# Kernel tuning notes

Measured on AMD Instinct MI355X. Metric: run time of the kernel, lower is better.

## Reference

```python
import jax, jax.numpy as jnp
import numpy as np
from functools import partial

B, D, E, O, K = 65536, 64, 16, 512, 2  # batch, feat dim, num_experts, output_size, top-k


def setup_inputs() -> dict:
    key = jax.random.key(0)
    k1, k2, k3, k4, k5 = jax.random.split(key, 5)
    scale_g = 1.0 / np.sqrt(D)
    return {
        "x": jax.random.normal(k1, (B, D), dtype=jnp.float32),
        "wg": jax.random.uniform(k2, (D, E), dtype=jnp.float32, minval=-scale_g, maxval=scale_g),
        "bg": jnp.zeros((E,), dtype=jnp.float32),
        "We": jax.random.uniform(k3, (E, D, O), dtype=jnp.float32, minval=-scale_g, maxval=scale_g),
        "be": jax.random.uniform(k4, (E, O), dtype=jnp.float32, minval=-scale_g, maxval=scale_g),
    }


def reference(x, wg, bg, We, be):
    # --- gating (noisy_gating=False / eval path) ---
    logits = jax.nn.softmax(x @ wg + bg, axis=1)            # [B, E]
    top_vals, top_idx = jax.lax.top_k(logits, K)            # [B, K]
    top_gates = top_vals / (jnp.sum(top_vals, axis=1, keepdims=True) + 1e-6)
    rows = jnp.arange(x.shape[0])[:, None]                  # [B, 1]
    gates = jnp.zeros_like(logits).at[rows, top_idx].set(top_gates)  # dense [B, E], sparse rows

    # --- dispatch / per-expert linear / gated scatter-combine ---
    # Equivalent dense-masked form of SparseDispatcher: y[i] = sum_e gates[i,e] * (x[i] @ We[e] + be[e])
    def step(y, ewb):
        w, b, g = ewb                                       # [D,O], [O], [B]
        return y + g[:, None] * (x @ w + b), None

    y0 = jnp.zeros((x.shape[0], We.shape[2]), dtype=x.dtype)
    y, _ = jax.lax.scan(step, y0, (We, be, gates.T))
    return y
```

## Files before the change

kernel.cpp:

```cpp
#include <hip/hip_runtime.h>

typedef unsigned int u32;
typedef unsigned short u16;
typedef float f4 __attribute__((ext_vector_type(4)));
typedef __bf16 b8 __attribute__((ext_vector_type(8)));
typedef unsigned short us8 __attribute__((ext_vector_type(8)));

#define DD 64
#define NE 16
#define OO 512
#define TR 64
#define MAXT 1344

struct __align__(16) Tile { u32 pid, slot, nr, pad; };

union U8 { us8 u; b8 b; };

__device__ __forceinline__ u16 f2bf(float f) {
  u32 u = __float_as_uint(f);
  u32 r = (u + 0x7fffu + ((u >> 16) & 1u)) >> 16;
  return (u16)r;
}

__global__ void k_wt(const float* __restrict__ We, u16* __restrict__ WeT) {
  __shared__ float tl[64][65];
  int b = blockIdx.x;
  int e = b >> 3;
  int oc = (b & 7) * 64;
  int t = threadIdx.x;
  int d = t >> 2, seg = (t & 3) * 16;
  const f4* src = (const f4*)(We + ((size_t)(e * DD + d)) * OO + oc + seg);
  f4 v0 = src[0], v1 = src[1], v2 = src[2], v3 = src[3];
#pragma unroll
  for (int j = 0; j < 4; j++) {
    tl[d][seg + j]      = v0[j];
    tl[d][seg + 4 + j]  = v1[j];
    tl[d][seg + 8 + j]  = v2[j];
    tl[d][seg + 12 + j] = v3[j];
  }
  __syncthreads();
  int o = t >> 2, ds = (t & 3) * 16;
  us8 o0, o1;
#pragma unroll
  for (int j = 0; j < 8; j++) {
    o0[j] = f2bf(tl[ds + j][o]);
    o1[j] = f2bf(tl[ds + 8 + j][o]);
  }
  u16* dst = WeT + ((size_t)(e * OO + oc + o)) * DD + ds;
  *(us8*)dst = o0;
  *(us8*)(dst + 8) = o1;
}

__global__ void k_gate(const float* __restrict__ x, const float* __restrict__ wg,
                       const float* __restrict__ bg, u32* __restrict__ hist,
                       u32* __restrict__ pid_arr, float* __restrict__ glo_arr,
                       float* __restrict__ ghi_arr) {
  __shared__ u32 hcnt[256];
  int t = threadIdx.x;
  hcnt[t] = 0;
  __syncthreads();
  int row = blockIdx.x * 256 + t;

  float l[NE];
#pragma unroll
  for (int e = 0; e < NE; e++) l[e] = bg[e];

  const f4* xp = (const f4*)(x + (size_t)row * DD);
  for (int d4 = 0; d4 < 16; d4++) {
    f4 xv = xp[d4];
#pragma unroll
    for (int qq = 0; qq < 4; qq++) {
      float xs = xv[qq];
      const float* wrow = wg + (d4 * 4 + qq) * NE;
#pragma unroll
      for (int e = 0; e < NE; e++) l[e] = fmaf(xs, wrow[e], l[e]);
    }
  }
  float mx = l[0];
#pragma unroll
  for (int e = 1; e < NE; e++) mx = fmaxf(mx, l[e]);
  float Z = 0.f;
#pragma unroll
  for (int e = 0; e < NE; e++) Z += __expf(l[e] - mx);
  int i1 = 0; float b1 = l[0];
#pragma unroll
  for (int e = 1; e < NE; e++) { if (l[e] > b1) { b1 = l[e]; i1 = e; } }
  int i2 = -1; float b2 = -1e30f;
#pragma unroll
  for (int e = 0; e < NE; e++) { if (e != i1 && l[e] > b2) { b2 = l[e]; i2 = e; } }
  float p1 = __expf(b1 - mx) / Z;
  float p2 = __expf(b2 - mx) / Z;
  float den = p1 + p2 + 1e-6f;
  float g1 = p1 / den, g2 = p2 / den;
  int elo, ehi; float glo, ghi;
  if (i1 < i2) { elo = i1; ehi = i2; glo = g1; ghi = g2; }
  else         { elo = i2; ehi = i1; glo = g2; ghi = g1; }
  u32 pid = (u32)(elo * NE + ehi);
  pid_arr[row] = pid;
  glo_arr[row] = glo;
  ghi_arr[row] = ghi;
  atomicAdd(&hcnt[pid], 1u);
  __syncthreads();
  hist[blockIdx.x * 256 + t] = hcnt[t];
}

__global__ void k_scan(u32* __restrict__ hist, u32* __restrict__ ntp,
                       Tile* __restrict__ tiles) {
  __shared__ u32 s[256], s2[256];
  int t = threadIdx.x;
  u32 total = 0;
  for (int b = 0; b < 256; b++) total += hist[b * 256 + t];
  u32 nt = (total + (TR - 1)) >> 6;
  s[t] = total; s2[t] = nt;
  __syncthreads();
  for (int d = 1; d < 256; d <<= 1) {
    u32 a = 0, c = 0;
    if (t >= d) { a = s[t - d]; c = s2[t - d]; }
    __syncthreads();
    s[t] += a; s2[t] += c;
    __syncthreads();
  }
  u32 base = s[t] - total;
  u32 tb   = s2[t] - nt;
  u32 run = base;
  for (int b = 0; b < 256; b++) {
    u32 v = hist[b * 256 + t];
    hist[b * 256 + t] = run;
    run += v;
  }
  for (u32 k = 0; k < nt; k++) {
    Tile td;
    td.pid = (u32)t;
    td.slot = base + k * (u32)TR;
    u32 rem = total - k * (u32)TR;
    td.nr = rem < (u32)TR ? rem : (u32)TR;
    td.pad = 0;
    tiles[tb + k] = td;
  }
  if (t == 255) *ntp = s2[255];
}

__global__ void k_scatter(const u32* __restrict__ pid_arr, const u32* __restrict__ hist,
                          u32* __restrict__ sorted) {
  __shared__ u32 lcnt[256];
  int t = threadIdx.x;
  lcnt[t] = 0;
  __syncthreads();
  int row = blockIdx.x * 256 + t;
  u32 pid = pid_arr[row];
  u32 rank = atomicAdd(&lcnt[pid], 1u);
  u32 off = hist[blockIdx.x * 256 + pid];
  sorted[off + rank] = (u32)row;
}

__global__ void k_moe(const float* __restrict__ x, const u16* __restrict__ WeT,
                      const float* __restrict__ be, const u32* __restrict__ sorted,
                      const u32* __restrict__ ntp, const Tile* __restrict__ tiles,
                      const float* __restrict__ glo_arr, const float* __restrict__ ghi_arr,
                      float* __restrict__ y) {
  __shared__ __align__(16) u16 Xl[TR * 72];
  __shared__ __align__(16) float Yl[TR * 68];
  __shared__ u32 rid_s[TR];
  __shared__ float glo_s[TR], ghi_s[TR];

  u32 bid = blockIdx.x;
  if (bid >= *ntp) return;
  Tile td = tiles[bid];
  u32 e_lo = td.pid >> 4, e_hi = td.pid & 15u;
  u32 slot0 = td.slot, nr = td.nr;

  int t = threadIdx.x;
  if (t < TR) {
    u32 i = (u32)t;
    u32 slot = slot0 + ((i < nr) ? i : 0u);
    u32 r = sorted[slot];
    rid_s[t] = r;
    bool valid = i < nr;
    glo_s[t] = valid ? glo_arr[r] : 0.f;
    ghi_s[t] = valid ? ghi_arr[r] : 0.f;
  }
  __syncthreads();
  {
    int i = t >> 2;
    int seg = (t & 3) * 16;
    u32 r = rid_s[i];
    const f4* xp = (const f4*)(x + (size_t)r * DD + seg);
    f4 v0 = xp[0], v1 = xp[1], v2 = xp[2], v3 = xp[3];
    float vv[16] = { v0[0], v0[1], v0[2], v0[3], v1[0], v1[1], v1[2], v1[3],
                     v2[0], v2[1], v2[2], v2[3], v3[0], v3[1], v3[2], v3[3] };
    us8 o0, o1;
#pragma unroll
    for (int j = 0; j < 8; j++) { o0[j] = f2bf(vv[j]); o1[j] = f2bf(vv[8 + j]); }
    *(us8*)&Xl[i * 72 + seg] = o0;
    *(us8*)&Xl[i * 72 + seg + 8] = o1;
  }
  __syncthreads();

  int lane = t & 63;
  int w = t >> 6;
  int q = lane >> 4;
  int ln = lane & 15;

  b8 afr[4][2];
#pragma unroll
  for (int mt = 0; mt < 4; mt++)
#pragma unroll
    for (int kc = 0; kc < 2; kc++) {
      U8 tmp; tmp.u = *(const us8*)&Xl[(mt * 16 + ln) * 72 + kc * 32 + q * 8];
      afr[mt][kc] = tmp.b;
    }

  float gl[16], gh[16];
#pragma unroll
  for (int mt = 0; mt < 4; mt++)
#pragma unroll
    for (int rr = 0; rr < 4; rr++) {
      int i = mt * 16 + q * 4 + rr;
      gl[mt * 4 + rr] = glo_s[i];
      gh[mt * 4 + rr] = ghi_s[i];
    }

  const u16* wlo = WeT + (size_t)e_lo * OO * DD;
  const u16* whi = WeT + (size_t)e_hi * OO * DD;
  const f4 zero = {0.f, 0.f, 0.f, 0.f};

  for (int jj = 0; jj < 8; jj++) {
    int col = jj * 64 + w * 16 + ln;
    const us8* plo = (const us8*)(wlo + (size_t)col * DD + q * 8);
    const us8* phi = (const us8*)(whi + (size_t)col * DD + q * 8);
    U8 t0, t1, t2, t3;
    t0.u = plo[0]; t1.u = plo[4];
    t2.u = phi[0]; t3.u = phi[4];
    b8 bl0 = t0.b, bl1 = t1.b, bh0 = t2.b, bh1 = t3.b;
    float blo = be[e_lo * OO + col];
    float bhi = be[e_hi * OO + col];

    f4 aL[4], aH[4];
#pragma unroll
    for (int mt = 0; mt < 4; mt++) { aL[mt] = zero; aH[mt] = zero; }
#pragma unroll
    for (int mt = 0; mt < 4; mt++) {
      aL[mt] = __builtin_amdgcn_mfma_f32_16x16x32_bf16(afr[mt][0], bl0, aL[mt], 0, 0, 0);
      aL[mt] = __builtin_amdgcn_mfma_f32_16x16x32_bf16(afr[mt][1], bl1, aL[mt], 0, 0, 0);
      aH[mt] = __builtin_amdgcn_mfma_f32_16x16x32_bf16(afr[mt][0], bh0, aH[mt], 0, 0, 0);
      aH[mt] = __builtin_amdgcn_mfma_f32_16x16x32_bf16(afr[mt][1], bh1, aH[mt], 0, 0, 0);
    }
#pragma unroll
    for (int mt = 0; mt < 4; mt++)
#pragma unroll
      for (int rr = 0; rr < 4; rr++) {
        int i = mt * 16 + q * 4 + rr;
        int idx = mt * 4 + rr;
        float v = gl[idx] * (aL[mt][rr] + blo) + gh[idx] * (aH[mt][rr] + bhi);
        Yl[i * 68 + w * 16 + ln] = v;
      }
    __syncthreads();
    {
      int row = t >> 2;
      int cs = (t & 3) * 16;
      if ((u32)row < nr) {
        float* yp = y + (size_t)rid_s[row] * OO + jj * 64 + cs;
        const float* sp = &Yl[row * 68 + cs];
#pragma unroll
        for (int u2 = 0; u2 < 4; u2++)
          *(f4*)(yp + u2 * 4) = *(const f4*)(sp + u2 * 4);
      }
    }
    __syncthreads();
  }
}

extern "C" void kernel_launch(void* const* d_in, const int* in_sizes, int n_in,
                              void* d_out, int out_size, void* d_ws, size_t ws_size,
                              hipStream_t stream) {
  const float* x  = (const float*)d_in[0];
  const float* wg = (const float*)d_in[1];
  const float* bg = (const float*)d_in[2];
  const float* We = (const float*)d_in[3];
  const float* be = (const float*)d_in[4];
  float* y = (float*)d_out;

  char* ws = (char*)d_ws;
  u32* ntp     = (u32*)(ws + 2048);
  Tile* tiles  = (Tile*)(ws + 4096);
  u32* pid_arr = (u32*)(ws + 32768);
  float* glo_a = (float*)(ws + 32768 + 262144);
  float* ghi_a = (float*)(ws + 32768 + 2 * 262144);
  u32* sorted  = (u32*)(ws + 32768 + 3 * 262144);
  u16* WeT     = (u16*)(ws + 32768 + 4 * 262144);
  u32* hist    = (u32*)(ws + 32768 + 4 * 262144 + 1048576);

  k_wt<<<128, 256, 0, stream>>>(We, WeT);
  k_gate<<<256, 256, 0, stream>>>(x, wg, bg, hist, pid_arr, glo_a, ghi_a);
  k_scan<<<1, 256, 0, stream>>>(hist, ntp, tiles);
  k_scatter<<<256, 256, 0, stream>>>(pid_arr, hist, sorted);
  k_moe<<<1144, 256, 0, stream>>>(x, WeT, be, sorted, ntp, tiles, glo_a, ghi_a, y);
}
```

Before: 217.4 us.

## Parallelize histogram prefix scan across blocks and widen output row stores

The single-block scan, which serially walked 256 histogram rows per thread twice, is split into a 256-block column scan kernel and a small single-block kernel that scans the per-pair totals and emits tiles. The scatter kernel then adds the per-pair base to the per-block offset. The final output copy in the MoE kernel is reorganized so 8 threads cover one 64-column row, giving contiguous 128-byte segments per row instead of 16-float strips. This adds one kernel launch and a strided column read in exchange for removing the serial scan latency.

```diff
diff --git a/kernel.cpp b/kernel.cpp
--- a/kernel.cpp
+++ b/kernel.cpp
@@ -10,7 +10,6 @@
 #define NE 16
 #define OO 512
 #define TR 64
-#define MAXT 1344
 
 struct __align__(16) Tile { u32 pid, slot, nr, pad; };
 
@@ -104,14 +103,30 @@
   hist[blockIdx.x * 256 + t] = hcnt[t];
 }
 
-__global__ void k_scan(u32* __restrict__ hist, u32* __restrict__ ntp,
-                       Tile* __restrict__ tiles) {
+__global__ void k_colscan(u32* __restrict__ hist, u32* __restrict__ tot) {
+  __shared__ u32 s[256];
+  int b = threadIdx.x, p = blockIdx.x;
+  u32 v = hist[b * 256 + p];
+  s[b] = v;
+  __syncthreads();
+  for (int d = 1; d < 256; d <<= 1) {
+    u32 a = 0;
+    if (b >= d) a = s[b - d];
+    __syncthreads();
+    s[b] += a;
+    __syncthreads();
+  }
+  hist[b * 256 + p] = s[b] - v;
+  if (b == 255) tot[p] = s[255];
+}
+
+__global__ void k_base(const u32* __restrict__ tot, u32* __restrict__ base,
+                       u32* __restrict__ ntp, Tile* __restrict__ tiles) {
   __shared__ u32 s[256], s2[256];
   int t = threadIdx.x;
-  u32 total = 0;
-  for (int b = 0; b < 256; b++) total += hist[b * 256 + t];
-  u32 nt = (total + (TR - 1)) >> 6;
-  s[t] = total; s2[t] = nt;
+  u32 v = tot[t];
+  u32 nt = (v + (TR - 1)) >> 6;
+  s[t] = v; s2[t] = nt;
   __syncthreads();
   for (int d = 1; d < 256; d <<= 1) {
     u32 a = 0, c = 0;
@@ -120,19 +135,14 @@
     s[t] += a; s2[t] += c;
     __syncthreads();
   }
-  u32 base = s[t] - total;
-  u32 tb   = s2[t] - nt;
-  u32 run = base;
-  for (int b = 0; b < 256; b++) {
-    u32 v = hist[b * 256 + t];
-    hist[b * 256 + t] = run;
-    run += v;
-  }
+  u32 rb = s[t] - v;
+  u32 tb = s2[t] - nt;
+  base[t] = rb;
   for (u32 k = 0; k < nt; k++) {
     Tile td;
     td.pid = (u32)t;
-    td.slot = base + k * (u32)TR;
-    u32 rem = total - k * (u32)TR;
+    td.slot = rb + k * (u32)TR;
+    u32 rem = v - k * (u32)TR;
     td.nr = rem < (u32)TR ? rem : (u32)TR;
     td.pad = 0;
     tiles[tb + k] = td;
@@ -141,15 +151,16 @@
 }
 
 __global__ void k_scatter(const u32* __restrict__ pid_arr, const u32* __restrict__ hist,
-                          u32* __restrict__ sorted) {
-  __shared__ u32 lcnt[256];
+                          const u32* __restrict__ base, u32* __restrict__ sorted) {
+  __shared__ u32 lcnt[256], lbase[256];
   int t = threadIdx.x;
   lcnt[t] = 0;
+  lbase[t] = base[t];
   __syncthreads();
   int row = blockIdx.x * 256 + t;
   u32 pid = pid_arr[row];
   u32 rank = atomicAdd(&lcnt[pid], 1u);
-  u32 off = hist[blockIdx.x * 256 + pid];
+  u32 off = lbase[pid] + hist[blockIdx.x * 256 + pid];
   sorted[off + rank] = (u32)row;
 }
 
@@ -256,14 +267,17 @@
       }
     __syncthreads();
     {
-      int row = t >> 2;
-      int cs = (t & 3) * 16;
-      if ((u32)row < nr) {
-        float* yp = y + (size_t)rid_s[row] * OO + jj * 64 + cs;
-        const float* sp = &Yl[row * 68 + cs];
-#pragma unroll
-        for (int u2 = 0; u2 < 4; u2++)
-          *(f4*)(yp + u2 * 4) = *(const f4*)(sp + u2 * 4);
+      int row0 = t >> 3;
+      int c8 = (t & 7) * 4;
+#pragma unroll
+      for (int half = 0; half < 2; half++) {
+        int row = half * 32 + row0;
+        if ((u32)row < nr) {
+          float* yp = y + (size_t)rid_s[row] * OO + jj * 64;
+          const float* sp = &Yl[row * 68];
+          *(f4*)(yp + c8)      = *(const f4*)(sp + c8);
+          *(f4*)(yp + 32 + c8) = *(const f4*)(sp + 32 + c8);
+        }
       }
     }
     __syncthreads();
@@ -281,7 +295,7 @@
   float* y = (float*)d_out;
 
   char* ws = (char*)d_ws;
-  u32* ntp     = (u32*)(ws + 2048);
+  u32* ntp     = (u32*)(ws + 0);
   Tile* tiles  = (Tile*)(ws + 4096);
   u32* pid_arr = (u32*)(ws + 32768);
   float* glo_a = (float*)(ws + 32768 + 262144);
@@ -289,10 +303,13 @@
   u32* sorted  = (u32*)(ws + 32768 + 3 * 262144);
   u16* WeT     = (u16*)(ws + 32768 + 4 * 262144);
   u32* hist    = (u32*)(ws + 32768 + 4 * 262144 + 1048576);
+  u32* tot     = (u32*)(ws + 32768 + 4 * 262144 + 1048576 + 262144);
+  u32* base    = (u32*)(ws + 32768 + 4 * 262144 + 1048576 + 262144 + 1024);
 
   k_wt<<<128, 256, 0, stream>>>(We, WeT);
   k_gate<<<256, 256, 0, stream>>>(x, wg, bg, hist, pid_arr, glo_a, ghi_a);
-  k_scan<<<1, 256, 0, stream>>>(hist, ntp, tiles);
-  k_scatter<<<256, 256, 0, stream>>>(pid_arr, hist, sorted);
+  k_colscan<<<256, 256, 0, stream>>>(hist, tot);
+  k_base<<<1, 256, 0, stream>>>(tot, base, ntp, tiles);
+  k_scatter<<<256, 256, 0, stream>>>(pid_arr, hist, base, sorted);
   k_moe<<<1144, 256, 0, stream>>>(x, WeT, be, sorted, ntp, tiles, glo_a, ghi_a, y);
 }
```

New measurement: 193.8 us. 10.8% less time.
